# Kernel tuning notes

Hardware: AMD Instinct MI355X
Metric: run time of the kernel (lower is better)

Reference implementation:

```python
import jax, jax.numpy as jnp
import numpy as np
from jax import lax

LOOKBACK = 336
N_FEATURES = 164
HORIZON = 96
D_MODEL = 64
D_STATE = 16
D_CONV = 4
EXPAND = 2
D_INNER = EXPAND * D_MODEL  # 128
DT_RANK = (D_MODEL + 15) // 16  # 4
MLP_HIDDEN = 64
BATCH = 512


def setup_inputs() -> dict:
    key = jax.random.key(0)
    ks = jax.random.split(key, 20)
    f32 = jnp.float32
    inp = {}
    inp["x_raw"] = jax.random.normal(ks[0], (BATCH, LOOKBACK), f32)
    inp["x_features"] = jax.random.normal(ks[1], (BATCH, N_FEATURES), f32)
    # embed Linear(1, d_model)
    inp["embed_W"] = jax.random.normal(ks[2], (1, D_MODEL), f32) * 0.5
    inp["embed_b"] = jnp.zeros((D_MODEL,), f32)
    # Mamba params (mamba-ssm layout, stored as [in, out] for matmul)
    inp["in_W"] = jax.random.normal(ks[3], (D_MODEL, 2 * D_INNER), f32) * (1.0 / np.sqrt(D_MODEL))
    inp["conv_W"] = jax.random.normal(ks[4], (D_INNER, D_CONV), f32) * 0.3
    inp["conv_b"] = jnp.zeros((D_INNER,), f32)
    inp["xproj_W"] = jax.random.normal(ks[5], (D_INNER, DT_RANK + 2 * D_STATE), f32) * (1.0 / np.sqrt(D_INNER))
    inp["dt_W"] = jax.random.normal(ks[6], (DT_RANK, D_INNER), f32) * (1.0 / np.sqrt(DT_RANK))
    inp["dt_b"] = jax.random.uniform(ks[7], (D_INNER,), f32, -4.0, -2.0)  # softplus -> small dt
    # A_log init = log(arange(1..d_state)) broadcast over d_inner, as in mamba-ssm
    inp["A_log"] = jnp.log(jnp.broadcast_to(jnp.arange(1, D_STATE + 1, dtype=f32), (D_INNER, D_STATE)))
    inp["D"] = jnp.ones((D_INNER,), f32)
    inp["out_W"] = jax.random.normal(ks[8], (D_INNER, D_MODEL), f32) * (1.0 / np.sqrt(D_INNER))
    # MLP stream
    inp["mlp_W1"] = jax.random.normal(ks[9], (N_FEATURES, MLP_HIDDEN), f32) * (1.0 / np.sqrt(N_FEATURES))
    inp["mlp_b1"] = jnp.zeros((MLP_HIDDEN,), f32)
    inp["mlp_W2"] = jax.random.normal(ks[10], (MLP_HIDDEN, MLP_HIDDEN // 2), f32) * (1.0 / np.sqrt(MLP_HIDDEN))
    inp["mlp_b2"] = jnp.zeros((MLP_HIDDEN // 2,), f32)
    # prediction head
    fin = D_MODEL + MLP_HIDDEN // 2
    inp["head_W"] = jax.random.normal(ks[11], (fin, HORIZON), f32) * (1.0 / np.sqrt(fin))
    inp["head_b"] = jnp.zeros((HORIZON,), f32)
    return inp


def silu(x):
    return x * jax.nn.sigmoid(x)


def mamba_block(u, in_W, conv_W, conv_b, xproj_W, dt_W, dt_b, A_log, D, out_W):
    # u: [B, L, d_model]
    B_, L, _ = u.shape
    xz = u @ in_W                      # [B, L, 2*D_INNER]
    x, z = jnp.split(xz, 2, axis=-1)   # each [B, L, D_INNER]
    # causal depthwise conv1d (pad left d_conv-1), then SiLU
    xc = x.transpose(0, 2, 1)          # [B, D_INNER, L]
    kern = conv_W[:, None, :]          # [D_INNER, 1, K] (OIH)
    xc = lax.conv_general_dilated(xc, kern, window_strides=(1,),
                                  padding=[(D_CONV - 1, 0)],
                                  dimension_numbers=("NCH", "OIH", "NCH"),
                                  feature_group_count=D_INNER)
    xc = silu(xc + conv_b[None, :, None])
    x = xc.transpose(0, 2, 1)          # [B, L, D_INNER]
    # input-dependent SSM params
    x_dbl = x @ xproj_W                # [B, L, DT_RANK + 2*D_STATE]
    dt = x_dbl[..., :DT_RANK]
    Bm = x_dbl[..., DT_RANK:DT_RANK + D_STATE]          # [B, L, N]
    Cm = x_dbl[..., DT_RANK + D_STATE:]                 # [B, L, N]
    delta = jax.nn.softplus(dt @ dt_W + dt_b)           # [B, L, D_INNER]
    A = -jnp.exp(A_log)                                 # [D_INNER, N]

    # selective scan over time
    def step(h, inps):
        d_t, B_t, C_t, x_t = inps  # [B,Di], [B,N], [B,N], [B,Di]
        dA = jnp.exp(d_t[:, :, None] * A[None])              # [B, Di, N]
        dBx = (d_t * x_t)[:, :, None] * B_t[:, None, :]      # [B, Di, N]
        h = dA * h + dBx
        y_t = jnp.einsum("bdn,bn->bd", h, C_t)
        return h, y_t

    h0 = jnp.zeros((B_, D_INNER, D_STATE), u.dtype)
    seq = (delta.transpose(1, 0, 2), Bm.transpose(1, 0, 2),
           Cm.transpose(1, 0, 2), x.transpose(1, 0, 2))
    _, ys = lax.scan(step, h0, seq)        # ys: [L, B, D_INNER]
    y = ys.transpose(1, 0, 2) + x * D[None, None, :]
    y = y * silu(z)
    return y @ out_W                        # [B, L, d_model]


def reference(x_raw, x_features, embed_W, embed_b, in_W, conv_W, conv_b,
              xproj_W, dt_W, dt_b, A_log, D, out_W,
              mlp_W1, mlp_b1, mlp_W2, mlp_b2, head_W, head_b):
    # embed raw series: [B, L] -> [B, L, 1] -> [B, L, d_model]
    h = x_raw[..., None] @ embed_W + embed_b
    h = mamba_block(h, in_W, conv_W, conv_b, xproj_W, dt_W, dt_b, A_log, D, out_W)
    h_mamba_out = h[:, -1, :]                       # [B, d_model]
    h_mlp = jax.nn.relu(x_features @ mlp_W1 + mlp_b1) @ mlp_W2 + mlp_b2
    h_final = jnp.concatenate([h_mamba_out, h_mlp], axis=1)
    return h_final @ head_W + head_b                # [B, horizon]
```

## Files before the change

kernel.cpp:

```cpp
#include <hip/hip_runtime.h>
#include <math.h>

#define LOOKBACK 336
#define NFEAT    164
#define HORIZON  96
#define DMODEL   64
#define DSTATE   16
#define DINNER   128
#define MLPH     64
#define BATCH    512
#define XCP      132
#define NGL      2
#define GSEG     84
#define CHK      12
#define NCH      7
#define HSTR     20
#define WSB      4480

typedef float v2f __attribute__((ext_vector_type(2)));

__device__ __forceinline__ float fast_rcp(float x) { return __builtin_amdgcn_rcpf(x); }
__device__ __forceinline__ float silu_f(float x) {
    return x * fast_rcp(1.f + __expf(-x));
}

__global__ __launch_bounds__(256, 2) void mamba_scan2(
    const float* __restrict__ x_raw,
    const float* __restrict__ embed_W, const float* __restrict__ embed_b,
    const float* __restrict__ in_W,
    const float* __restrict__ conv_W,  const float* __restrict__ conv_b,
    const float* __restrict__ xproj_W, const float* __restrict__ dt_W,
    const float* __restrict__ dt_b,    const float* __restrict__ A_log,
    float* __restrict__ ws)
{
    __shared__ __align__(16) float xrl[172];
    __shared__ __align__(16) float xprojT[20*XCP];
    __shared__ __align__(16) float xcbuf[2][NGL][CHK*XCP];
    __shared__ __align__(16) float Bsh[NGL][CHK][DSTATE];
    __shared__ __align__(16) float dtraw[NGL][CHK][4];

    const int tid   = threadIdx.x;
    const int batch = blockIdx.x >> 1;
    const int half  = blockIdx.x & 1;
    const int gl    = tid >> 7;
    const int ch    = tid & 127;

    for (int i = tid; i < 171; i += 256) {
        int t = half*168 + i - 3;
        xrl[i] = (t >= 0) ? x_raw[batch*LOOKBACK + t] : 0.f;
    }
    for (int idx = tid; idx < 20*DINNER; idx += 256) {
        int jj = idx >> 7, d = idx & 127;
        xprojT[jj*XCP + d] = xproj_W[d*36 + jj];
    }

    float w1 = 0.f, w0 = 0.f;
    for (int dm = 0; dm < DMODEL; ++dm) {
        float w = in_W[dm*(2*DINNER) + ch];
        w1 = fmaf(embed_W[dm], w, w1);
        w0 = fmaf(embed_b[dm], w, w0);
    }
    const float4 cw = *(const float4*)&conv_W[ch*4];
    const float  cb = conv_b[ch];
    const float dtw0 = dt_W[ch],       dtw1 = dt_W[128 + ch],
                dtw2 = dt_W[256 + ch], dtw3 = dt_W[384 + ch];
    const float dtb_r = dt_b[ch];
    bool structured = true;
    #pragma unroll
    for (int i = 0; i < 16; ++i) {
        float a = __expf(A_log[ch*DSTATE + i]);
        float ex = (float)(i + 1);
        structured = structured && (fabsf(a - ex) < 1e-3f * ex);
    }
    const bool sfast = __all(structured);

    const int a2jp = tid / 12;
    const int a2tt = tid - a2jp*12;
    const int cch = tid & 127;
    __syncthreads();

    {
        float* xw = &xcbuf[0][gl][0];
        const float* xr = &xrl[gl*GSEG];
        if (half == 0 && gl == 0) {
            for (int tt = 0; tt < CHK; ++tt) {
                float acc = cb;
                if (tt >= 3) acc = fmaf(fmaf(xr[tt],   w1, w0), cw.x, acc);
                if (tt >= 2) acc = fmaf(fmaf(xr[tt+1], w1, w0), cw.y, acc);
                if (tt >= 1) acc = fmaf(fmaf(xr[tt+2], w1, w0), cw.z, acc);
                acc = fmaf(fmaf(xr[tt+3], w1, w0), cw.w, acc);
                xw[tt*XCP + ch] = silu_f(acc);
            }
        } else {
            float e0 = fmaf(xr[0], w1, w0);
            float e1 = fmaf(xr[1], w1, w0);
            float e2 = fmaf(xr[2], w1, w0);
            #pragma unroll
            for (int tt = 0; tt < CHK; ++tt) {
                float e3 = fmaf(xr[tt+3], w1, w0);
                float acc = cb + e0*cw.x + e1*cw.y + e2*cw.z + e3*cw.w;
                xw[tt*XCP + ch] = silu_f(acc);
                e0 = e1; e1 = e2; e2 = e3;
            }
        }
    }
    __syncthreads();

    v2f h01={0,0},h23={0,0},h45={0,0},h67={0,0},
        h89={0,0},hAB={0,0},hCD={0,0},hEF={0,0};
    float dacc = 0.f;

    for (int c = 0; c < NCH; ++c) {
        const int buf = c & 1;

        if (tid < 120) {
            const int j0 = a2jp*2;
            const float* p0  = &xprojT[j0*XCP];
            const float* p1  = &xprojT[(j0+1)*XCP];
            const float* xra = &xcbuf[buf][0][a2tt*XCP];
            const float* xrb = &xcbuf[buf][1][a2tt*XCP];
            v2f a0a={0,0}, a1a={0,0}, a0b={0,0}, a1b={0,0};
            #pragma unroll 4
            for (int d = 0; d < DINNER; d += 4) {
                float4 q0 = *(const float4*)(p0 + d);
                float4 q1 = *(const float4*)(p1 + d);
                float4 xa = *(const float4*)(xra + d);
                float4 xb = *(const float4*)(xrb + d);
                v2f q0l={q0.x,q0.y}, q0h={q0.z,q0.w};
                v2f q1l={q1.x,q1.y}, q1h={q1.z,q1.w};
                v2f xal={xa.x,xa.y}, xah={xa.z,xa.w};
                v2f xbl={xb.x,xb.y}, xbh={xb.z,xb.w};
                a0a = __builtin_elementwise_fma(xal, q0l, a0a);
                a0a = __builtin_elementwise_fma(xah, q0h, a0a);
                a1a = __builtin_elementwise_fma(xal, q1l, a1a);
                a1a = __builtin_elementwise_fma(xah, q1h, a1a);
                a0b = __builtin_elementwise_fma(xbl, q0l, a0b);
                a0b = __builtin_elementwise_fma(xbh, q0h, a0b);
                a1b = __builtin_elementwise_fma(xbl, q1l, a1b);
                a1b = __builtin_elementwise_fma(xbh, q1h, a1b);
            }
            float r0a=a0a.x+a0a.y, r1a=a1a.x+a1a.y;
            float r0b=a0b.x+a0b.y, r1b=a1b.x+a1b.y;
            if (j0 < 4) {
                *(float2*)&dtraw[0][a2tt][j0] = make_float2(r0a, r1a);
                *(float2*)&dtraw[1][a2tt][j0] = make_float2(r0b, r1b);
            } else {
                *(float2*)&Bsh[0][a2tt][j0-4] = make_float2(r0a, r1a);
                *(float2*)&Bsh[1][a2tt][j0-4] = make_float2(r0b, r1b);
            }
        } else if (tid >= 128 && c + 1 < NCH) {
            #pragma unroll
            for (int q = 0; q < 2; ++q) {
                float* xw = &xcbuf[buf^1][q][0];
                const float* xr = &xrl[q*GSEG + (c+1)*CHK];
                float e0 = fmaf(xr[0], w1, w0);
                float e1 = fmaf(xr[1], w1, w0);
                float e2 = fmaf(xr[2], w1, w0);
                float v = 0.f;
                #pragma unroll
                for (int tt = 0; tt < CHK; ++tt) {
                    float e3 = fmaf(xr[tt+3], w1, w0);
                    float acc = cb + e0*cw.x + e1*cw.y + e2*cw.z + e3*cw.w;
                    v = silu_f(acc);
                    xw[tt*XCP + cch] = v;
                    e0 = e1; e1 = e2; e2 = e3;
                }
                if (half == 1 && q == 1 && c + 1 == NCH-1)
                    ws[(size_t)batch*WSB + 4352 + cch] = v;
            }
        }
        __syncthreads();

        const float* xs = &xcbuf[buf][gl][0];
        if (__builtin_expect(sfast, 1)) {
            #pragma unroll
            for (int tt = 0; tt < CHK; ++tt) {
                float4 dr = *(const float4*)&dtraw[gl][tt][0];
                float dv = fmaf(dr.x, dtw0, fmaf(dr.y, dtw1,
                           fmaf(dr.z, dtw2, fmaf(dr.w, dtw3, dtb_r))));
                float e  = __expf(dv);
                float p  = 1.f + e;
                float r  = fast_rcp(p);
                float dl = (dv > 80.f) ? dv : __logf(p);
                dacc += dl;
                float ux = dl * xs[tt*XCP + ch];
                float4 B0 = *(const float4*)&Bsh[gl][tt][0];
                float4 B1 = *(const float4*)&Bsh[gl][tt][4];
                float4 B2 = *(const float4*)&Bsh[gl][tt][8];
                float4 B3 = *(const float4*)&Bsh[gl][tt][12];
                float r2 = r*r, r4 = r2*r2, r8 = r4*r4;
                v2f r2v = {r2, r2}, r4v = {r4, r4}, r8v = {r8, r8};
                v2f p01 = {r, r2};
                v2f p23 = p01*r2v;
                v2f p45 = p01*r4v, p67 = p23*r4v;
                v2f p89 = p01*r8v, pAB = p23*r8v, pCD = p45*r8v, pEF = p67*r8v;
                v2f uxv = {ux, ux};
                h01 = __builtin_elementwise_fma(p01, h01, uxv*(v2f){B0.x,B0.y});
                h23 = __builtin_elementwise_fma(p23, h23, uxv*(v2f){B0.z,B0.w});
                h45 = __builtin_elementwise_fma(p45, h45, uxv*(v2f){B1.x,B1.y});
                h67 = __builtin_elementwise_fma(p67, h67, uxv*(v2f){B1.z,B1.w});
                h89 = __builtin_elementwise_fma(p89, h89, uxv*(v2f){B2.x,B2.y});
                hAB = __builtin_elementwise_fma(pAB, hAB, uxv*(v2f){B2.z,B2.w});
                hCD = __builtin_elementwise_fma(pCD, hCD, uxv*(v2f){B3.x,B3.y});
                hEF = __builtin_elementwise_fma(pEF, hEF, uxv*(v2f){B3.z,B3.w});
            }
        } else {
            const float* Arow = A_log + ch*DSTATE;
            for (int tt = 0; tt < CHK; ++tt) {
                float4 dr = *(const float4*)&dtraw[gl][tt][0];
                float dv = fmaf(dr.x, dtw0, fmaf(dr.y, dtw1,
                           fmaf(dr.z, dtw2, fmaf(dr.w, dtw3, dtb_r))));
                float e  = __expf(dv);
                float dl = (dv > 15.f) ? dv : __logf(1.f + e);
                dacc += dl;
                float ux = dl * xs[tt*XCP + ch];
                const float* Brow = &Bsh[gl][tt][0];
                float hv[16] = {h01.x,h01.y,h23.x,h23.y,h45.x,h45.y,h67.x,h67.y,
                                h89.x,h89.y,hAB.x,hAB.y,hCD.x,hCD.y,hEF.x,hEF.y};
                for (int i = 0; i < 16; ++i)
                    hv[i] = fmaf(__expf(-__expf(Arow[i])*dl), hv[i], ux*Brow[i]);
                h01=(v2f){hv[0],hv[1]};   h23=(v2f){hv[2],hv[3]};
                h45=(v2f){hv[4],hv[5]};   h67=(v2f){hv[6],hv[7]};
                h89=(v2f){hv[8],hv[9]};   hAB=(v2f){hv[10],hv[11]};
                hCD=(v2f){hv[12],hv[13]}; hEF=(v2f){hv[14],hv[15]};
            }
        }
        __syncthreads();
    }

    float* hpart = &xcbuf[0][0][0];
    float* dsum  = &Bsh[0][0][0];
    if (gl == 0) {
        float4* hp = (float4*)&hpart[ch*HSTR];
        hp[0] = make_float4(h01.x,h01.y,h23.x,h23.y);
        hp[1] = make_float4(h45.x,h45.y,h67.x,h67.y);
        hp[2] = make_float4(h89.x,h89.y,hAB.x,hAB.y);
        hp[3] = make_float4(hCD.x,hCD.y,hEF.x,hEF.y);
        dsum[ch] = dacc;
    }
    __syncthreads();
    if (gl == 1) {
        const float4* hp = (const float4*)&hpart[ch*HSTR];
        float4 a = hp[0], bq = hp[1], cq = hp[2], dq = hp[3];
        float h0[16] = {a.x,a.y,a.z,a.w,bq.x,bq.y,bq.z,bq.w,
                        cq.x,cq.y,cq.z,cq.w,dq.x,dq.y,dq.z,dq.w};
        float h1[16] = {h01.x,h01.y,h23.x,h23.y,h45.x,h45.y,h67.x,h67.y,
                        h89.x,h89.y,hAB.x,hAB.y,hCD.x,hCD.y,hEF.x,hEF.y};
        float P[16];
        if (structured) {
            float r = __expf(-dacc);
            float pw = 1.f;
            #pragma unroll
            for (int i = 0; i < 16; ++i) { pw *= r; P[i] = fmaf(pw, h0[i], h1[i]); }
        } else {
            #pragma unroll
            for (int i = 0; i < 16; ++i)
                P[i] = fmaf(__expf(-__expf(A_log[ch*DSTATE+i])*dacc), h0[i], h1[i]);
        }
        float* wsb = ws + (size_t)batch*WSB + half*2176;
        float4* pw4 = (float4*)(wsb + ch*16);
        pw4[0] = make_float4(P[0],P[1],P[2],P[3]);
        pw4[1] = make_float4(P[4],P[5],P[6],P[7]);
        pw4[2] = make_float4(P[8],P[9],P[10],P[11]);
        pw4[3] = make_float4(P[12],P[13],P[14],P[15]);
        wsb[2048 + ch] = dsum[ch] + dacc;
    }
}

__global__ __launch_bounds__(128, 2) void mamba_epi(
    const float* __restrict__ x_raw,   const float* __restrict__ x_features,
    const float* __restrict__ embed_W, const float* __restrict__ embed_b,
    const float* __restrict__ in_W,    const float* __restrict__ xproj_W,
    const float* __restrict__ A_log,   const float* __restrict__ Dvec,
    const float* __restrict__ out_W,
    const float* __restrict__ mlp_W1,  const float* __restrict__ mlp_b1,
    const float* __restrict__ mlp_W2,  const float* __restrict__ mlp_b2,
    const float* __restrict__ head_W,  const float* __restrict__ head_b,
    const float* __restrict__ ws,      float* __restrict__ out)
{
    __shared__ float xcl[DINNER], Cpart[8][16], Cl[DSTATE], yv[DINNER];
    __shared__ float hfin[96], mlph[MLPH];

    const int ch = threadIdx.x;
    const int b  = blockIdx.x;
    const float* wsb = ws + (size_t)b*WSB;

    xcl[ch] = wsb[4352 + ch];

    bool structured = true;
    #pragma unroll
    for (int i = 0; i < 16; ++i) {
        float a = __expf(A_log[ch*DSTATE + i]);
        float ex = (float)(i + 1);
        structured = structured && (fabsf(a - ex) < 1e-3f * ex);
    }

    float H[16];
    {
        const float4* p01 = (const float4*)(wsb + ch*16);
        const float4* p23 = (const float4*)(wsb + 2176 + ch*16);
        float D23 = wsb[2176 + 2048 + ch];
        float4 a0 = p01[0], a1 = p01[1], a2 = p01[2], a3 = p01[3];
        float4 b0 = p23[0], b1 = p23[1], b2 = p23[2], b3 = p23[3];
        float P0[16] = {a0.x,a0.y,a0.z,a0.w,a1.x,a1.y,a1.z,a1.w,
                        a2.x,a2.y,a2.z,a2.w,a3.x,a3.y,a3.z,a3.w};
        float P1[16] = {b0.x,b0.y,b0.z,b0.w,b1.x,b1.y,b1.z,b1.w,
                        b2.x,b2.y,b2.z,b2.w,b3.x,b3.y,b3.z,b3.w};
        if (structured) {
            float r = __expf(-D23);
            float pw = 1.f;
            #pragma unroll
            for (int i = 0; i < 16; ++i) { pw *= r; H[i] = fmaf(pw, P0[i], P1[i]); }
        } else {
            #pragma unroll
            for (int i = 0; i < 16; ++i)
                H[i] = fmaf(__expf(-__expf(A_log[ch*DSTATE+i])*D23), P0[i], P1[i]);
        }
    }

    float zs;
    {
        float a1 = 0.f, a0 = 0.f;
        for (int dm = 0; dm < DMODEL; ++dm) {
            float w = in_W[dm*(2*DINNER) + DINNER + ch];
            a1 = fmaf(embed_W[dm], w, a1);
            a0 = fmaf(embed_b[dm], w, a0);
        }
        zs = silu_f(fmaf(x_raw[b*LOOKBACK + 335], a1, a0));
    }
    __syncthreads();

    {
        const int q = ch >> 4, n = ch & 15;
        float acc = 0.f;
        for (int d = q*16; d < q*16 + 16; ++d)
            acc = fmaf(xcl[d], xproj_W[d*36 + 20 + n], acc);
        Cpart[q][n] = acc;
    }
    __syncthreads();

    if (ch < 16) {
        float s = 0.f;
        #pragma unroll
        for (int q = 0; q < 8; ++q) s += Cpart[q][ch];
        Cl[ch] = s;
    } else if (ch >= 64) {
        const int j = ch - 64;
        const float* xf = x_features + b*NFEAT;
        float acc = 0.f;
        for (int f = 0; f < NFEAT; ++f)
            acc = fmaf(xf[f], mlp_W1[f*MLPH + j], acc);
        mlph[j] = fmaxf(acc + mlp_b1[j], 0.f);
    }
    __syncthreads();

    {
        float acc = 0.f;
        #pragma unroll
        for (int i = 0; i < 16; ++i) acc = fmaf(H[i], Cl[i], acc);
        float y = acc + xcl[ch]*Dvec[ch];
        yv[ch] = y * zs;
    }
    __syncthreads();

    {
        const int o = ch >> 1, k = ch & 1;
        float acc = 0.f;
        for (int d = k*64; d < k*64 + 64; ++d)
            acc = fmaf(yv[d], out_W[d*DMODEL + o], acc);
        acc += __shfl_xor(acc, 1);
        if (k == 0) hfin[o] = acc;
    }
    __syncthreads();

    if (ch < 64) {
        const int j = ch >> 1, k = ch & 1;
        float acc = 0.f;
        for (int kk = k*32; kk < k*32 + 32; ++kk)
            acc = fmaf(mlph[kk], mlp_W2[kk*32 + j], acc);
        acc += __shfl_xor(acc, 1);
        if (k == 0) hfin[64 + j] = acc + mlp_b2[j];
    }
    __syncthreads();

    if (ch < HORIZON) {
        float acc = 0.f;
        for (int i = 0; i < 96; ++i)
            acc = fmaf(hfin[i], head_W[i*HORIZON + ch], acc);
        out[b*HORIZON + ch] = acc + head_b[ch];
    }
}

extern "C" void kernel_launch(void* const* d_in, const int* in_sizes, int n_in,
                              void* d_out, int out_size, void* d_ws, size_t ws_size,
                              hipStream_t stream) {
    (void)in_sizes; (void)n_in; (void)out_size; (void)ws_size;
    float* ws = (float*)d_ws;
    mamba_scan2<<<BATCH*2, 256, 0, stream>>>(
        (const float*)d_in[0],
        (const float*)d_in[2],  (const float*)d_in[3],  (const float*)d_in[4],
        (const float*)d_in[5],  (const float*)d_in[6],  (const float*)d_in[7],
        (const float*)d_in[8],  (const float*)d_in[9],  (const float*)d_in[10],
        ws);
    mamba_epi<<<BATCH, 128, 0, stream>>>(
        (const float*)d_in[0],  (const float*)d_in[1],  (const float*)d_in[2],
        (const float*)d_in[3],  (const float*)d_in[4],  (const float*)d_in[7],
        (const float*)d_in[10], (const float*)d_in[11], (const float*)d_in[12],
        (const float*)d_in[13], (const float*)d_in[14], (const float*)d_in[15],
        (const float*)d_in[16], (const float*)d_in[17], (const float*)d_in[18],
        ws, (float*)d_out);
}
```

Measured before the change: 176.3 us.

## Move z-gate, MLP layer-1 and C projection into scan kernel tail; widen epilogue

Moves the z-gate silu, the first MLP layer and the last-step C projection out of the epilogue kernel. They now run at the end of the scan kernel, split by half across the two blocks per batch, and write to new workspace slots. The epilogue is reduced to the state combine, out projection, MLP layer 2 and head. It now runs with 256 threads and splits each reduction over more lanes to shorten its serial dependency chains. This trades a longer scan-kernel tail and extra global round-trips for a lighter epilogue.

```diff
diff --git a/kernel.cpp b/kernel.cpp
--- a/kernel.cpp
+++ b/kernel.cpp
@@ -15,7 +15,7 @@
 #define CHK      12
 #define NCH      7
 #define HSTR     20
-#define WSB      4480
+#define WSB      4736
 
 typedef float v2f __attribute__((ext_vector_type(2)));
 
@@ -25,12 +25,13 @@
 }
 
 __global__ __launch_bounds__(256, 2) void mamba_scan2(
-    const float* __restrict__ x_raw,
+    const float* __restrict__ x_raw,   const float* __restrict__ x_features,
     const float* __restrict__ embed_W, const float* __restrict__ embed_b,
     const float* __restrict__ in_W,
     const float* __restrict__ conv_W,  const float* __restrict__ conv_b,
     const float* __restrict__ xproj_W, const float* __restrict__ dt_W,
     const float* __restrict__ dt_b,    const float* __restrict__ A_log,
+    const float* __restrict__ mlp_W1,  const float* __restrict__ mlp_b1,
     float* __restrict__ ws)
 {
     __shared__ __align__(16) float xrl[172];
@@ -38,6 +39,7 @@
     __shared__ __align__(16) float xcbuf[2][NGL][CHK*XCP];
     __shared__ __align__(16) float Bsh[NGL][CHK][DSTATE];
     __shared__ __align__(16) float dtraw[NGL][CHK][4];
+    __shared__ __align__(16) float xcl_lds[DINNER];
 
     const int tid   = threadIdx.x;
     const int batch = blockIdx.x >> 1;
@@ -165,8 +167,10 @@
                     xw[tt*XCP + cch] = v;
                     e0 = e1; e1 = e2; e2 = e3;
                 }
-                if (half == 1 && q == 1 && c + 1 == NCH-1)
+                if (half == 1 && q == 1 && c + 1 == NCH-1) {
                     ws[(size_t)batch*WSB + 4352 + cch] = v;
+                    xcl_lds[cch] = v;
+                }
             }
         }
         __syncthreads();
@@ -230,6 +234,7 @@
 
     float* hpart = &xcbuf[0][0][0];
     float* dsum  = &Bsh[0][0][0];
+    float* Cpart = &Bsh[0][0][0] + 128;
     if (gl == 0) {
         float4* hp = (float4*)&hpart[ch*HSTR];
         hp[0] = make_float4(h01.x,h01.y,h23.x,h23.y);
@@ -265,38 +270,69 @@
         pw4[3] = make_float4(P[12],P[13],P[14],P[15]);
         wsb[2048 + ch] = dsum[ch] + dacc;
     }
+
+    if (half == 0) {
+        if (tid < 128) {
+            float a1 = 0.f, a0 = 0.f;
+            for (int dm = 0; dm < DMODEL; ++dm) {
+                float w = in_W[dm*(2*DINNER) + DINNER + tid];
+                a1 = fmaf(embed_W[dm], w, a1);
+                a0 = fmaf(embed_b[dm], w, a0);
+            }
+            float x335 = x_raw[batch*LOOKBACK + 335];
+            ws[(size_t)batch*WSB + 4480 + tid] = silu_f(fmaf(x335, a1, a0));
+        } else {
+            const int lane = tid - 128;
+            const int j = lane >> 1, k = lane & 1;
+            const float* xf = x_features + batch*NFEAT;
+            float acc = 0.f;
+            const int f0 = k*82, f1 = (k ? NFEAT : 82);
+            for (int f = f0; f < f1; ++f)
+                acc = fmaf(xf[f], mlp_W1[f*MLPH + j], acc);
+            acc += __shfl_xor(acc, 1);
+            if (k == 0)
+                ws[(size_t)batch*WSB + 4608 + j] = fmaxf(acc + mlp_b1[j], 0.f);
+        }
+    } else {
+        if (tid < 128) {
+            const int q = tid >> 4, n = tid & 15;
+            float acc = 0.f;
+            for (int d = q*16; d < q*16 + 16; ++d)
+                acc = fmaf(xcl_lds[d], xproj_W[d*36 + 20 + n], acc);
+            Cpart[q*16 + n] = acc;
+        }
+        __syncthreads();
+        if (tid < 16) {
+            float s = 0.f;
+            #pragma unroll
+            for (int q = 0; q < 8; ++q) s += Cpart[q*16 + tid];
+            ws[(size_t)batch*WSB + 4672 + tid] = s;
+        }
+    }
 }
 
-__global__ __launch_bounds__(128, 2) void mamba_epi(
-    const float* __restrict__ x_raw,   const float* __restrict__ x_features,
-    const float* __restrict__ embed_W, const float* __restrict__ embed_b,
-    const float* __restrict__ in_W,    const float* __restrict__ xproj_W,
+__global__ __launch_bounds__(256, 2) void mamba_epi(
     const float* __restrict__ A_log,   const float* __restrict__ Dvec,
     const float* __restrict__ out_W,
-    const float* __restrict__ mlp_W1,  const float* __restrict__ mlp_b1,
     const float* __restrict__ mlp_W2,  const float* __restrict__ mlp_b2,
     const float* __restrict__ head_W,  const float* __restrict__ head_b,
     const float* __restrict__ ws,      float* __restrict__ out)
 {
-    __shared__ float xcl[DINNER], Cpart[8][16], Cl[DSTATE], yv[DINNER];
-    __shared__ float hfin[96], mlph[MLPH];
-
-    const int ch = threadIdx.x;
-    const int b  = blockIdx.x;
+    __shared__ float yv[DINNER], hfin[96];
+
+    const int tid = threadIdx.x;
+    const int b   = blockIdx.x;
     const float* wsb = ws + (size_t)b*WSB;
 
-    xcl[ch] = wsb[4352 + ch];
-
-    bool structured = true;
-    #pragma unroll
-    for (int i = 0; i < 16; ++i) {
-        float a = __expf(A_log[ch*DSTATE + i]);
-        float ex = (float)(i + 1);
-        structured = structured && (fabsf(a - ex) < 1e-3f * ex);
-    }
-
-    float H[16];
-    {
+    if (tid < 128) {
+        const int ch = tid;
+        bool structured = true;
+        #pragma unroll
+        for (int i = 0; i < 16; ++i) {
+            float a = __expf(A_log[ch*DSTATE + i]);
+            float ex = (float)(i + 1);
+            structured = structured && (fabsf(a - ex) < 1e-3f * ex);
+        }
         const float4* p01 = (const float4*)(wsb + ch*16);
         const float4* p23 = (const float4*)(wsb + 2176 + ch*16);
         float D23 = wsb[2176 + 2048 + ch];
@@ -306,6 +342,7 @@
                         a2.x,a2.y,a2.z,a2.w,a3.x,a3.y,a3.z,a3.w};
         float P1[16] = {b0.x,b0.y,b0.z,b0.w,b1.x,b1.y,b1.z,b1.w,
                         b2.x,b2.y,b2.z,b2.w,b3.x,b3.y,b3.z,b3.w};
+        float H[16];
         if (structured) {
             float r = __expf(-D23);
             float pw = 1.f;
@@ -316,78 +353,43 @@
             for (int i = 0; i < 16; ++i)
                 H[i] = fmaf(__expf(-__expf(A_log[ch*DSTATE+i])*D23), P0[i], P1[i]);
         }
-    }
-
-    float zs;
-    {
-        float a1 = 0.f, a0 = 0.f;
-        for (int dm = 0; dm < DMODEL; ++dm) {
-            float w = in_W[dm*(2*DINNER) + DINNER + ch];
-            a1 = fmaf(embed_W[dm], w, a1);
-            a0 = fmaf(embed_b[dm], w, a0);
-        }
-        zs = silu_f(fmaf(x_raw[b*LOOKBACK + 335], a1, a0));
-    }
-    __syncthreads();
-
-    {
-        const int q = ch >> 4, n = ch & 15;
-        float acc = 0.f;
-        for (int d = q*16; d < q*16 + 16; ++d)
-            acc = fmaf(xcl[d], xproj_W[d*36 + 20 + n], acc);
-        Cpart[q][n] = acc;
-    }
-    __syncthreads();
-
-    if (ch < 16) {
-        float s = 0.f;
-        #pragma unroll
-        for (int q = 0; q < 8; ++q) s += Cpart[q][ch];
-        Cl[ch] = s;
-    } else if (ch >= 64) {
-        const int j = ch - 64;
-        const float* xf = x_features + b*NFEAT;
-        float acc = 0.f;
-        for (int f = 0; f < NFEAT; ++f)
-            acc = fmaf(xf[f], mlp_W1[f*MLPH + j], acc);
-        mlph[j] = fmaxf(acc + mlp_b1[j], 0.f);
-    }
-    __syncthreads();
-
-    {
+        const float* Cl = wsb + 4672;
         float acc = 0.f;
         #pragma unroll
         for (int i = 0; i < 16; ++i) acc = fmaf(H[i], Cl[i], acc);
-        float y = acc + xcl[ch]*Dvec[ch];
-        yv[ch] = y * zs;
+        float y = acc + wsb[4352 + ch]*Dvec[ch];
+        yv[ch] = y * wsb[4480 + ch];
+    } else {
+        const int lane = tid - 128;
+        const int j = lane >> 2, k = lane & 3;
+        const float* mlph = wsb + 4608;
+        float acc = 0.f;
+        for (int kk = k*16; kk < k*16 + 16; ++kk)
+            acc = fmaf(mlph[kk], mlp_W2[kk*32 + j], acc);
+        acc += __shfl_xor(acc, 1);
+        acc += __shfl_xor(acc, 2);
+        if (k == 0) hfin[64 + j] = acc + mlp_b2[j];
     }
     __syncthreads();
 
     {
-        const int o = ch >> 1, k = ch & 1;
+        const int o = tid >> 2, k = tid & 3;
         float acc = 0.f;
-        for (int d = k*64; d < k*64 + 64; ++d)
+        for (int d = k*32; d < k*32 + 32; ++d)
             acc = fmaf(yv[d], out_W[d*DMODEL + o], acc);
         acc += __shfl_xor(acc, 1);
+        acc += __shfl_xor(acc, 2);
         if (k == 0) hfin[o] = acc;
     }
     __syncthreads();
 
-    if (ch < 64) {
-        const int j = ch >> 1, k = ch & 1;
+    if (tid < 192) {
+        const int o = tid >> 1, k = tid & 1;
         float acc = 0.f;
-        for (int kk = k*32; kk < k*32 + 32; ++kk)
-            acc = fmaf(mlph[kk], mlp_W2[kk*32 + j], acc);
+        for (int i = k*48; i < k*48 + 48; ++i)
+            acc = fmaf(hfin[i], head_W[i*HORIZON + o], acc);
         acc += __shfl_xor(acc, 1);
-        if (k == 0) hfin[64 + j] = acc + mlp_b2[j];
-    }
-    __syncthreads();
-
-    if (ch < HORIZON) {
-        float acc = 0.f;
-        for (int i = 0; i < 96; ++i)
-            acc = fmaf(hfin[i], head_W[i*HORIZON + ch], acc);
-        out[b*HORIZON + ch] = acc + head_b[ch];
+        if (k == 0) out[b*HORIZON + o] = acc + head_b[o];
     }
 }
 
@@ -397,16 +399,14 @@
     (void)in_sizes; (void)n_in; (void)out_size; (void)ws_size;
     float* ws = (float*)d_ws;
     mamba_scan2<<<BATCH*2, 256, 0, stream>>>(
-        (const float*)d_in[0],
+        (const float*)d_in[0],  (const float*)d_in[1],
         (const float*)d_in[2],  (const float*)d_in[3],  (const float*)d_in[4],
         (const float*)d_in[5],  (const float*)d_in[6],  (const float*)d_in[7],
         (const float*)d_in[8],  (const float*)d_in[9],  (const float*)d_in[10],
+        (const float*)d_in[13], (const float*)d_in[14],
         ws);
-    mamba_epi<<<BATCH, 128, 0, stream>>>(
-        (const float*)d_in[0],  (const float*)d_in[1],  (const float*)d_in[2],
-        (const float*)d_in[3],  (const float*)d_in[4],  (const float*)d_in[7],
+    mamba_epi<<<BATCH, 256, 0, stream>>>(
         (const float*)d_in[10], (const float*)d_in[11], (const float*)d_in[12],
-        (const float*)d_in[13], (const float*)d_in[14], (const float*)d_in[15],
-        (const float*)d_in[16], (const float*)d_in[17], (const float*)d_in[18],
-        ws, (float*)d_out);
+        (const float*)d_in[15], (const float*)d_in[16], (const float*)d_in[17],
+        (const float*)d_in[18], ws, (float*)d_out);
 }
```

Result: no change. 173.0 us (-1.9%).
